# Optimization experiments

Measured on AMD Instinct MI355X. Metric: run time of the kernel, lower is better.

Reference implementation:

```python
import jax, jax.numpy as jnp
import numpy as np

NEG = -10000.0  # fp16-safe mask value, as in the torch module


def prelu(x, a):
    # nn.PReLU() default: single learnable slope shared across channels
    return jnp.where(x >= 0, x, a * x)


def setup_inputs() -> dict:
    key = jax.random.key(0)
    ks = jax.random.split(key, 9)
    B, L, D = 2048, 200, 128
    H1, H2 = 256, 128
    query = jax.random.normal(ks[0], (B, D), dtype=jnp.float32)
    keys = jax.random.normal(ks[1], (B, L, D), dtype=jnp.float32)
    mask = jax.random.randint(ks[2], (B, L), 0, 2, dtype=jnp.int32)
    s1 = 1.0 / np.sqrt(4 * D)
    s2 = 1.0 / np.sqrt(H1)
    s3 = 1.0 / np.sqrt(H2)
    W1 = jax.random.uniform(ks[3], (H1, 4 * D), minval=-s1, maxval=s1, dtype=jnp.float32)
    b1 = jax.random.uniform(ks[4], (H1,), minval=-s1, maxval=s1, dtype=jnp.float32)
    W2 = jax.random.uniform(ks[5], (H2, H1), minval=-s2, maxval=s2, dtype=jnp.float32)
    b2 = jax.random.uniform(ks[6], (H2,), minval=-s2, maxval=s2, dtype=jnp.float32)
    W3 = jax.random.uniform(ks[7], (1, H2), minval=-s3, maxval=s3, dtype=jnp.float32)
    b3 = jax.random.uniform(ks[8], (1,), minval=-s3, maxval=s3, dtype=jnp.float32)
    a1 = jnp.asarray(0.25, dtype=jnp.float32)  # PReLU init
    a2 = jnp.asarray(0.25, dtype=jnp.float32)
    return {"query": query, "keys": keys, "mask": mask,
            "W1": W1, "b1": b1, "a1": a1, "W2": W2, "b2": b2, "a2": a2,
            "W3": W3, "b3": b3}


def reference(query, keys, mask, W1, b1, a1, W2, b2, a2, W3, b3):
    B, L, D = keys.shape
    q = jnp.broadcast_to(query[:, None, :], (B, L, D))
    # [B, L, 4D] concat feature (query, key, diff, product)
    att_in = jnp.concatenate([q, keys, q - keys, q * keys], axis=-1)
    h = prelu(jnp.einsum('blf,hf->blh', att_in, W1) + b1, a1)
    h = prelu(jnp.einsum('blh,gh->blg', h, W2) + b2, a2)
    scores = (jnp.einsum('blg,og->blo', h, W3) + b3)[..., 0]  # [B, L]
    scores = jnp.where(mask == 0, NEG, scores)
    w = jax.nn.softmax(scores, axis=-1)
    w = jnp.where(mask == 0, 0.0, w)
    # weighted sum over history -> user interest [B, D]
    return jnp.einsum('bl,bld->bd', w, keys)
```

## Files before the change

kernel.cpp:

```cpp
#include <hip/hip_runtime.h>
#include <hip/hip_bf16.h>
#include <cstdint>

#define NEGV (-10000.0f)

typedef short bf16x8 __attribute__((ext_vector_type(8)));
typedef short bf16x4 __attribute__((ext_vector_type(4)));
typedef float f32x4 __attribute__((ext_vector_type(4)));

__device__ __forceinline__ short f2bf(float f) {
  union { float f; uint32_t u; } v; v.f = f;
  uint32_t u = v.u + 0x7fffu + ((v.u >> 16) & 1u);
  return (short)(u >> 16);
}
__device__ __forceinline__ float b2f(short s) {
  union { uint32_t u; float f; } v; v.u = ((uint32_t)(uint16_t)s) << 16;
  return v.f;
}
__device__ __forceinline__ uint32_t pk2(float lo, float hi) {
  union { __hip_bfloat162 h2; uint32_t u; } cv;
  cv.h2.x = __float2bfloat16(lo);
  cv.h2.y = __float2bfloat16(hi);
  return cv.u;
}

__global__ void prep_weights(const float* __restrict__ W1, const float* __restrict__ W2,
                             short* __restrict__ Wk, short* __restrict__ Wd,
                             short* __restrict__ W2b) {
  int idx = blockIdx.x * 256 + threadIdx.x;
  if (idx < 32768) {
    int h = idx >> 7, d = idx & 127;
    Wk[idx] = f2bf(W1[h * 512 + 128 + d] - W1[h * 512 + 256 + d]);
  } else if (idx < 65536) {
    int i = idx - 32768;
    int h = i >> 7, d = i & 127;
    Wd[i] = f2bf(W1[h * 512 + 384 + d]);
  } else {
    int i = idx - 65536;
    W2b[i] = f2bf(W2[i]);
  }
}

__global__ void prep_u(const float* __restrict__ query, const float* __restrict__ W1,
                       const float* __restrict__ b1, float* __restrict__ U) {
  __shared__ float q8[8][128];
  int tid = threadIdx.x;
  int b0 = blockIdx.x * 8;
  for (int i = tid; i < 1024; i += 256)
    q8[i >> 7][i & 127] = query[(size_t)(b0 + (i >> 7)) * 128 + (i & 127)];
  __syncthreads();
  int h = tid;
  const float4* w0 = (const float4*)(W1 + (size_t)h * 512);
  const float4* w1 = (const float4*)(W1 + (size_t)h * 512 + 256);
  float acc[8];
  float bb = b1[h];
#pragma unroll
  for (int i = 0; i < 8; ++i) acc[i] = bb;
  for (int d4 = 0; d4 < 32; ++d4) {
    float4 wa = w0[d4], wb = w1[d4];
    float wv0 = wa.x + wb.x, wv1 = wa.y + wb.y, wv2 = wa.z + wb.z, wv3 = wa.w + wb.w;
#pragma unroll
    for (int i = 0; i < 8; ++i) {
      float4 qv = ((const float4*)q8[i])[d4];
      acc[i] += wv0 * qv.x + wv1 * qv.y + wv2 * qv.z + wv3 * qv.w;
    }
  }
#pragma unroll
  for (int i = 0; i < 8; ++i) U[(size_t)(b0 + i) * 256 + h] = acc[i];
}

__global__ __launch_bounds__(256, 2) void din_scores(
    const float* __restrict__ query, const float* __restrict__ keys,
    const float* __restrict__ b2p, const float* __restrict__ a1p,
    const float* __restrict__ a2p, const float* __restrict__ W3,
    const float* __restrict__ U, const short* __restrict__ Wk,
    const short* __restrict__ Wd, const short* __restrict__ W2b,
    float* __restrict__ scores_g) {
  __shared__ short Kt[2][16 * 128];
  __shared__ short H1[2][16 * 256];
  __shared__ float wred[4][208];
  __shared__ float Ul[256];
  __shared__ float b2l[128];
  __shared__ float w3l[128];

  const int tid = threadIdx.x;
  const int b = blockIdx.x;
  const int lane = tid & 63, wid = tid >> 6;
  const int lr = lane & 15, lg = lane >> 4;

  const float a1 = a1p[0], a2 = a2p[0];

  Ul[tid] = U[(size_t)b * 256 + tid];
  if (tid < 128) { b2l[tid] = b2p[tid]; w3l[tid] = W3[tid]; }

  bf16x8 mf[4][4];
  {
    const float* qrow = query + (size_t)b * 128;
#pragma unroll
    for (int nt = 0; nt < 4; ++nt) {
      int h = wid * 64 + nt * 16 + lr;
#pragma unroll
      for (int ks = 0; ks < 4; ++ks) {
        int d0 = ks * 32 + lg * 8;
        bf16x8 wk = *(const bf16x8*)(Wk + h * 128 + d0);
        bf16x8 wd = *(const bf16x8*)(Wd + h * 128 + d0);
        float4 q0 = *(const float4*)(qrow + d0);
        float4 q1 = *(const float4*)(qrow + d0 + 4);
        float qv[8] = {q0.x, q0.y, q0.z, q0.w, q1.x, q1.y, q1.z, q1.w};
        float mv[8];
#pragma unroll
        for (int j = 0; j < 8; ++j) mv[j] = b2f(wk[j]) + b2f(wd[j]) * qv[j];
        union { bf16x8 v; uint32_t u[4]; } mm;
#pragma unroll
        for (int j = 0; j < 4; ++j) mm.u[j] = pk2(mv[2 * j], mv[2 * j + 1]);
        mf[nt][ks] = mm.v;
      }
    }
  }
  bf16x8 w2f[2][8];
#pragma unroll
  for (int nt2 = 0; nt2 < 2; ++nt2) {
    int g = wid * 32 + nt2 * 16 + lr;
#pragma unroll
    for (int ks = 0; ks < 8; ++ks)
      w2f[nt2][ks] = *(const bf16x8*)(W2b + g * 256 + ks * 32 + lg * 8);
  }

  const int srow = tid >> 4;
  const int scol = (tid & 15) * 8;
  const int ssw = (srow & 7) << 3;

  {
    const float4* kp4 = (const float4*)(keys + ((size_t)b * 200 + srow) * 128 + scol);
    float4 s0 = kp4[0], s1 = kp4[1];
    union { bf16x8 v; uint32_t u[4]; } w;
    w.u[0] = pk2(s0.x, s0.y); w.u[1] = pk2(s0.z, s0.w);
    w.u[2] = pk2(s1.x, s1.y); w.u[3] = pk2(s1.z, s1.w);
    *(bf16x8*)(&Kt[0][srow * 128 + (scol ^ ssw)]) = w.v;
  }
  __syncthreads();

  for (int t = 0; t < 13; ++t) {
    const int buf = t & 1;

    float4 st0, st1;
    if (t < 12) {
      int gl = (t + 1) * 16 + srow;
      st0 = st1 = make_float4(0.f, 0.f, 0.f, 0.f);
      if (gl < 200) {
        const float4* kp4 = (const float4*)(keys + ((size_t)b * 200 + gl) * 128 + scol);
        st0 = kp4[0]; st1 = kp4[1];
      }
    }

    const int sw = (lr & 7) << 3;
    bf16x8 kf[4];
#pragma unroll
    for (int ks = 0; ks < 4; ++ks)
      kf[ks] = *(const bf16x8*)(&Kt[buf][lr * 128 + ((ks * 32 + lg * 8) ^ sw)]);
    f32x4 acc[4];
#pragma unroll
    for (int nt = 0; nt < 4; ++nt)
#pragma unroll
      for (int r = 0; r < 4; ++r) acc[nt][r] = Ul[wid * 64 + nt * 16 + lg * 4 + r];
    __builtin_amdgcn_s_setprio(1);
#pragma unroll
    for (int ks = 0; ks < 4; ++ks)
#pragma unroll
      for (int nt = 0; nt < 4; ++nt)
        acc[nt] = __builtin_amdgcn_mfma_f32_16x16x32_bf16(mf[nt][ks], kf[ks], acc[nt], 0, 0, 0);
    __builtin_amdgcn_s_setprio(0);
    short* h1b = H1[buf];
#pragma unroll
    for (int nt = 0; nt < 4; ++nt) {
      float v0 = acc[nt][0], v1 = acc[nt][1], v2 = acc[nt][2], v3 = acc[nt][3];
      v0 = (v0 >= 0.f) ? v0 : a1 * v0;
      v1 = (v1 >= 0.f) ? v1 : a1 * v1;
      v2 = (v2 >= 0.f) ? v2 : a1 * v2;
      v3 = (v3 >= 0.f) ? v3 : a1 * v3;
      union { bf16x4 v; uint32_t u[2]; } hh;
      hh.u[0] = pk2(v0, v1); hh.u[1] = pk2(v2, v3);
      int h0 = wid * 64 + nt * 16 + lg * 4;
      *(bf16x4*)(&h1b[lr * 256 + (h0 ^ sw)]) = hh.v;
    }

    if (t < 12) {
      union { bf16x8 v; uint32_t u[4]; } w;
      w.u[0] = pk2(st0.x, st0.y); w.u[1] = pk2(st0.z, st0.w);
      w.u[2] = pk2(st1.x, st1.y); w.u[3] = pk2(st1.z, st1.w);
      *(bf16x8*)(&Kt[buf ^ 1][srow * 128 + (scol ^ ssw)]) = w.v;
    }
    __syncthreads();

    f32x4 acc2[2];
#pragma unroll
    for (int nt2 = 0; nt2 < 2; ++nt2)
#pragma unroll
      for (int r = 0; r < 4; ++r) acc2[nt2][r] = b2l[wid * 32 + nt2 * 16 + lg * 4 + r];
    __builtin_amdgcn_s_setprio(1);
#pragma unroll
    for (int ks = 0; ks < 8; ++ks) {
      bf16x8 hf = *(const bf16x8*)(&h1b[lr * 256 + ((ks * 32 + lg * 8) ^ sw)]);
      acc2[0] = __builtin_amdgcn_mfma_f32_16x16x32_bf16(w2f[0][ks], hf, acc2[0], 0, 0, 0);
      acc2[1] = __builtin_amdgcn_mfma_f32_16x16x32_bf16(w2f[1][ks], hf, acc2[1], 0, 0, 0);
    }
    __builtin_amdgcn_s_setprio(0);
    float s = 0.f;
#pragma unroll
    for (int nt2 = 0; nt2 < 2; ++nt2)
#pragma unroll
      for (int r = 0; r < 4; ++r) {
        float v = acc2[nt2][r];
        v = (v >= 0.f) ? v : a2 * v;
        s += v * w3l[wid * 32 + nt2 * 16 + lg * 4 + r];
      }
    s += __shfl_xor(s, 16);
    s += __shfl_xor(s, 32);
    if (lg == 0) wred[wid][t * 16 + lr] = s;
  }
  __syncthreads();

  if (tid < 200) {
    float s = wred[0][tid] + wred[1][tid] + wred[2][tid] + wred[3][tid];
    scores_g[(size_t)b * 200 + tid] = s;
  }
}

__global__ __launch_bounds__(256) void din_wsum(
    const float* __restrict__ keys, const int* __restrict__ mask,
    const float* __restrict__ scores_g, float* __restrict__ out) {
  __shared__ float wl[208];
  __shared__ float red[8];
  __shared__ float opart[8][128];

  const int tid = threadIdx.x;
  const int b = blockIdx.x;
  const int lane = tid & 63, wid = tid >> 6;

  float val = NEGV;
  int mk = 0;
  if (tid < 200) {
    mk = mask[(size_t)b * 200 + tid];
    val = mk ? scores_g[(size_t)b * 200 + tid] : NEGV;
  }
  float m = val;
#pragma unroll
  for (int off = 1; off < 64; off <<= 1) m = fmaxf(m, __shfl_xor(m, off));
  if (lane == 0) red[wid] = m;
  __syncthreads();
  float smax = fmaxf(fmaxf(red[0], red[1]), fmaxf(red[2], red[3]));
  float pex = (tid < 200 && mk) ? __expf(val - smax) : 0.f;
  float s = pex;
#pragma unroll
  for (int off = 1; off < 64; off <<= 1) s += __shfl_xor(s, off);
  if (lane == 0) red[4 + wid] = s;
  __syncthreads();
  float ssum = red[4] + red[5] + red[6] + red[7];
  float winv = (ssum > 0.f) ? 1.f / ssum : 0.f;
  if (tid < 208) wl[tid] = (tid < 200) ? pex * winv : 0.f;
  __syncthreads();

  {
    const int d4 = (tid & 31) << 2;
    const int slice = tid >> 5;
    float ax = 0.f, ay = 0.f, az = 0.f, aw = 0.f;
    for (int l = slice; l < 200; l += 8) {
      float wv = wl[l];
      float4 kv = *(const float4*)(keys + ((size_t)b * 200 + l) * 128 + d4);
      ax += wv * kv.x; ay += wv * kv.y; az += wv * kv.z; aw += wv * kv.w;
    }
    *(float4*)(&opart[slice][d4]) = make_float4(ax, ay, az, aw);
  }
  __syncthreads();
  if (tid < 128) {
    float acc = 0.f;
#pragma unroll
    for (int i = 0; i < 8; ++i) acc += opart[i][tid];
    out[(size_t)b * 128 + tid] = acc;
  }
}

extern "C" void kernel_launch(void* const* d_in, const int* in_sizes, int n_in,
                              void* d_out, int out_size, void* d_ws, size_t ws_size,
                              hipStream_t stream) {
  const float* query = (const float*)d_in[0];
  const float* keys  = (const float*)d_in[1];
  const int*   maskp = (const int*)d_in[2];
  const float* W1    = (const float*)d_in[3];
  const float* b1    = (const float*)d_in[4];
  const float* a1    = (const float*)d_in[5];
  const float* W2    = (const float*)d_in[6];
  const float* b2    = (const float*)d_in[7];
  const float* a2    = (const float*)d_in[8];
  const float* W3    = (const float*)d_in[9];
  float* out = (float*)d_out;

  float* U        = (float*)d_ws;
  short* Wk       = (short*)((char*)d_ws + 2097152);
  short* Wd       = Wk + 32768;
  short* W2b      = Wd + 32768;
  float* scores_g = (float*)((char*)d_ws + 2097152 + 196608);

  prep_weights<<<384, 256, 0, stream>>>(W1, W2, Wk, Wd, W2b);
  prep_u<<<256, 256, 0, stream>>>(query, W1, b1, U);
  din_scores<<<2048, 256, 0, stream>>>(query, keys, b2, a1, a2, W3,
                                       U, Wk, Wd, W2b, scores_g);
  din_wsum<<<2048, 256, 0, stream>>>(keys, maskp, scores_g, out);
}
```

Before: 164.0 us.

## Split din_scores into layer-1 and layer-2 warp groups with software pipelining

The score kernel now runs 1024 threads per block: 8 waves compute the first MLP layer for tile t while 8 other waves compute layer 2 and the score reduction for tile t-1 and stage the next key tile. The two layers overlap across warp-specialized groups, which halves per-wave fragment registers and takes the layer-2 work off the layer-1 critical path. In exchange there is an extra pipeline phase, one barrier per phase across 16 waves, likely lower blocks-per-CU occupancy, and U/b2/W3 are read straight from global memory into registers.

```diff
diff --git a/kernel.cpp b/kernel.cpp
--- a/kernel.cpp
+++ b/kernel.cpp
@@ -69,7 +69,7 @@
   for (int i = 0; i < 8; ++i) U[(size_t)(b0 + i) * 256 + h] = acc[i];
 }
 
-__global__ __launch_bounds__(256, 2) void din_scores(
+__global__ __launch_bounds__(1024) void din_scores(
     const float* __restrict__ query, const float* __restrict__ keys,
     const float* __restrict__ b2p, const float* __restrict__ a1p,
     const float* __restrict__ a2p, const float* __restrict__ W3,
@@ -78,27 +78,25 @@
     float* __restrict__ scores_g) {
   __shared__ short Kt[2][16 * 128];
   __shared__ short H1[2][16 * 256];
-  __shared__ float wred[4][208];
-  __shared__ float Ul[256];
-  __shared__ float b2l[128];
-  __shared__ float w3l[128];
+  __shared__ float wred[8][208];
 
   const int tid = threadIdx.x;
   const int b = blockIdx.x;
   const int lane = tid & 63, wid = tid >> 6;
   const int lr = lane & 15, lg = lane >> 4;
-
-  const float a1 = a1p[0], a2 = a2p[0];
-
-  Ul[tid] = U[(size_t)b * 256 + tid];
-  if (tid < 128) { b2l[tid] = b2p[tid]; w3l[tid] = W3[tid]; }
-
-  bf16x8 mf[4][4];
-  {
+  const bool isG1 = wid < 8;
+
+  bf16x8 frag[8];
+  f32x4 accA, accB;
+  float uv0[4], uv1[4];
+  float alpha;
+
+  if (isG1) {
+    alpha = a1p[0];
     const float* qrow = query + (size_t)b * 128;
 #pragma unroll
-    for (int nt = 0; nt < 4; ++nt) {
-      int h = wid * 64 + nt * 16 + lr;
+    for (int nt = 0; nt < 2; ++nt) {
+      int h = wid * 32 + nt * 16 + lr;
 #pragma unroll
       for (int ks = 0; ks < 4; ++ks) {
         int d0 = ks * 32 + lg * 8;
@@ -113,115 +111,123 @@
         union { bf16x8 v; uint32_t u[4]; } mm;
 #pragma unroll
         for (int j = 0; j < 4; ++j) mm.u[j] = pk2(mv[2 * j], mv[2 * j + 1]);
-        mf[nt][ks] = mm.v;
+        frag[nt * 4 + ks] = mm.v;
       }
     }
-  }
-  bf16x8 w2f[2][8];
-#pragma unroll
-  for (int nt2 = 0; nt2 < 2; ++nt2) {
-    int g = wid * 32 + nt2 * 16 + lr;
+#pragma unroll
+    for (int r = 0; r < 4; ++r) {
+      uv0[r] = U[(size_t)b * 256 + wid * 32 + lg * 4 + r];
+      uv1[r] = U[(size_t)b * 256 + wid * 32 + 16 + lg * 4 + r];
+    }
+  } else {
+    alpha = a2p[0];
+    int g = (wid - 8) * 16 + lr;
 #pragma unroll
     for (int ks = 0; ks < 8; ++ks)
-      w2f[nt2][ks] = *(const bf16x8*)(W2b + g * 256 + ks * 32 + lg * 8);
-  }
-
-  const int srow = tid >> 4;
-  const int scol = (tid & 15) * 8;
+      frag[ks] = *(const bf16x8*)(W2b + g * 256 + ks * 32 + lg * 8);
+#pragma unroll
+    for (int r = 0; r < 4; ++r) {
+      int gg = (wid - 8) * 16 + lg * 4 + r;
+      uv0[r] = b2p[gg];
+      uv1[r] = W3[gg];
+    }
+  }
+
+  const int j = tid - 512;
+  const int srow = j >> 5;
+  const int scol = (j & 31) * 4;
   const int ssw = (srow & 7) << 3;
 
-  {
-    const float4* kp4 = (const float4*)(keys + ((size_t)b * 200 + srow) * 128 + scol);
-    float4 s0 = kp4[0], s1 = kp4[1];
-    union { bf16x8 v; uint32_t u[4]; } w;
-    w.u[0] = pk2(s0.x, s0.y); w.u[1] = pk2(s0.z, s0.w);
-    w.u[2] = pk2(s1.x, s1.y); w.u[3] = pk2(s1.z, s1.w);
-    *(bf16x8*)(&Kt[0][srow * 128 + (scol ^ ssw)]) = w.v;
-  }
-  __syncthreads();
-
-  for (int t = 0; t < 13; ++t) {
-    const int buf = t & 1;
-
-    float4 st0, st1;
-    if (t < 12) {
-      int gl = (t + 1) * 16 + srow;
-      st0 = st1 = make_float4(0.f, 0.f, 0.f, 0.f);
-      if (gl < 200) {
-        const float4* kp4 = (const float4*)(keys + ((size_t)b * 200 + gl) * 128 + scol);
-        st0 = kp4[0]; st1 = kp4[1];
+  if (!isG1) {
+    float4 st = *(const float4*)(keys + ((size_t)b * 200 + srow) * 128 + scol);
+    union { bf16x4 v; uint32_t u[2]; } w;
+    w.u[0] = pk2(st.x, st.y); w.u[1] = pk2(st.z, st.w);
+    *(bf16x4*)(&Kt[0][srow * 128 + (scol ^ ssw)]) = w.v;
+  }
+  __syncthreads();
+
+  const int sw = (lr & 7) << 3;
+
+  for (int ph = 0; ph < 14; ++ph) {
+    const int buf = ph & 1;
+
+    float4 st;
+    bool sv = false;
+    if (!isG1 && ph < 12) {
+      int gl = (ph + 1) * 16 + srow;
+      st = make_float4(0.f, 0.f, 0.f, 0.f);
+      sv = true;
+      if (gl < 200) st = *(const float4*)(keys + ((size_t)b * 200 + gl) * 128 + scol);
+    }
+
+    if (isG1) {
+      if (ph < 13) {
+        bf16x8 kf[4];
+#pragma unroll
+        for (int ks = 0; ks < 4; ++ks)
+          kf[ks] = *(const bf16x8*)(&Kt[buf][lr * 128 + ((ks * 32 + lg * 8) ^ sw)]);
+#pragma unroll
+        for (int r = 0; r < 4; ++r) { accA[r] = uv0[r]; accB[r] = uv1[r]; }
+        __builtin_amdgcn_s_setprio(1);
+#pragma unroll
+        for (int ks = 0; ks < 4; ++ks) {
+          accA = __builtin_amdgcn_mfma_f32_16x16x32_bf16(frag[ks], kf[ks], accA, 0, 0, 0);
+          accB = __builtin_amdgcn_mfma_f32_16x16x32_bf16(frag[4 + ks], kf[ks], accB, 0, 0, 0);
+        }
+        __builtin_amdgcn_s_setprio(0);
+        float v0, v1, v2, v3;
+        union { bf16x4 v; uint32_t u[2]; } hh;
+        v0 = accA[0]; v1 = accA[1]; v2 = accA[2]; v3 = accA[3];
+        v0 = (v0 >= 0.f) ? v0 : alpha * v0;
+        v1 = (v1 >= 0.f) ? v1 : alpha * v1;
+        v2 = (v2 >= 0.f) ? v2 : alpha * v2;
+        v3 = (v3 >= 0.f) ? v3 : alpha * v3;
+        hh.u[0] = pk2(v0, v1); hh.u[1] = pk2(v2, v3);
+        *(bf16x4*)(&H1[buf][lr * 256 + ((wid * 32 + lg * 4) ^ sw)]) = hh.v;
+        v0 = accB[0]; v1 = accB[1]; v2 = accB[2]; v3 = accB[3];
+        v0 = (v0 >= 0.f) ? v0 : alpha * v0;
+        v1 = (v1 >= 0.f) ? v1 : alpha * v1;
+        v2 = (v2 >= 0.f) ? v2 : alpha * v2;
+        v3 = (v3 >= 0.f) ? v3 : alpha * v3;
+        hh.u[0] = pk2(v0, v1); hh.u[1] = pk2(v2, v3);
+        *(bf16x4*)(&H1[buf][lr * 256 + ((wid * 32 + 16 + lg * 4) ^ sw)]) = hh.v;
       }
-    }
-
-    const int sw = (lr & 7) << 3;
-    bf16x8 kf[4];
-#pragma unroll
-    for (int ks = 0; ks < 4; ++ks)
-      kf[ks] = *(const bf16x8*)(&Kt[buf][lr * 128 + ((ks * 32 + lg * 8) ^ sw)]);
-    f32x4 acc[4];
-#pragma unroll
-    for (int nt = 0; nt < 4; ++nt)
-#pragma unroll
-      for (int r = 0; r < 4; ++r) acc[nt][r] = Ul[wid * 64 + nt * 16 + lg * 4 + r];
-    __builtin_amdgcn_s_setprio(1);
-#pragma unroll
-    for (int ks = 0; ks < 4; ++ks)
-#pragma unroll
-      for (int nt = 0; nt < 4; ++nt)
-        acc[nt] = __builtin_amdgcn_mfma_f32_16x16x32_bf16(mf[nt][ks], kf[ks], acc[nt], 0, 0, 0);
-    __builtin_amdgcn_s_setprio(0);
-    short* h1b = H1[buf];
-#pragma unroll
-    for (int nt = 0; nt < 4; ++nt) {
-      float v0 = acc[nt][0], v1 = acc[nt][1], v2 = acc[nt][2], v3 = acc[nt][3];
-      v0 = (v0 >= 0.f) ? v0 : a1 * v0;
-      v1 = (v1 >= 0.f) ? v1 : a1 * v1;
-      v2 = (v2 >= 0.f) ? v2 : a1 * v2;
-      v3 = (v3 >= 0.f) ? v3 : a1 * v3;
-      union { bf16x4 v; uint32_t u[2]; } hh;
-      hh.u[0] = pk2(v0, v1); hh.u[1] = pk2(v2, v3);
-      int h0 = wid * 64 + nt * 16 + lg * 4;
-      *(bf16x4*)(&h1b[lr * 256 + (h0 ^ sw)]) = hh.v;
-    }
-
-    if (t < 12) {
-      union { bf16x8 v; uint32_t u[4]; } w;
-      w.u[0] = pk2(st0.x, st0.y); w.u[1] = pk2(st0.z, st0.w);
-      w.u[2] = pk2(st1.x, st1.y); w.u[3] = pk2(st1.z, st1.w);
-      *(bf16x8*)(&Kt[buf ^ 1][srow * 128 + (scol ^ ssw)]) = w.v;
+    } else {
+      if (ph >= 1) {
+#pragma unroll
+        for (int r = 0; r < 4; ++r) accA[r] = uv0[r];
+        const short* h1b = H1[buf ^ 1];
+        __builtin_amdgcn_s_setprio(1);
+#pragma unroll
+        for (int ks = 0; ks < 8; ++ks) {
+          bf16x8 hf = *(const bf16x8*)(&h1b[lr * 256 + ((ks * 32 + lg * 8) ^ sw)]);
+          accA = __builtin_amdgcn_mfma_f32_16x16x32_bf16(frag[ks], hf, accA, 0, 0, 0);
+        }
+        __builtin_amdgcn_s_setprio(0);
+        float s = 0.f;
+#pragma unroll
+        for (int r = 0; r < 4; ++r) {
+          float v = accA[r];
+          v = (v >= 0.f) ? v : alpha * v;
+          s += v * uv1[r];
+        }
+        s += __shfl_xor(s, 16);
+        s += __shfl_xor(s, 32);
+        if (lg == 0) wred[wid - 8][(ph - 1) * 16 + lr] = s;
+      }
+      if (sv) {
+        union { bf16x4 v; uint32_t u[2]; } w;
+        w.u[0] = pk2(st.x, st.y); w.u[1] = pk2(st.z, st.w);
+        *(bf16x4*)(&Kt[buf ^ 1][srow * 128 + (scol ^ ssw)]) = w.v;
+      }
     }
     __syncthreads();
-
-    f32x4 acc2[2];
-#pragma unroll
-    for (int nt2 = 0; nt2 < 2; ++nt2)
-#pragma unroll
-      for (int r = 0; r < 4; ++r) acc2[nt2][r] = b2l[wid * 32 + nt2 * 16 + lg * 4 + r];
-    __builtin_amdgcn_s_setprio(1);
-#pragma unroll
-    for (int ks = 0; ks < 8; ++ks) {
-      bf16x8 hf = *(const bf16x8*)(&h1b[lr * 256 + ((ks * 32 + lg * 8) ^ sw)]);
-      acc2[0] = __builtin_amdgcn_mfma_f32_16x16x32_bf16(w2f[0][ks], hf, acc2[0], 0, 0, 0);
-      acc2[1] = __builtin_amdgcn_mfma_f32_16x16x32_bf16(w2f[1][ks], hf, acc2[1], 0, 0, 0);
-    }
-    __builtin_amdgcn_s_setprio(0);
+  }
+
+  if (tid < 200) {
     float s = 0.f;
 #pragma unroll
-    for (int nt2 = 0; nt2 < 2; ++nt2)
-#pragma unroll
-      for (int r = 0; r < 4; ++r) {
-        float v = acc2[nt2][r];
-        v = (v >= 0.f) ? v : a2 * v;
-        s += v * w3l[wid * 32 + nt2 * 16 + lg * 4 + r];
-      }
-    s += __shfl_xor(s, 16);
-    s += __shfl_xor(s, 32);
-    if (lg == 0) wred[wid][t * 16 + lr] = s;
-  }
-  __syncthreads();
-
-  if (tid < 200) {
-    float s = wred[0][tid] + wred[1][tid] + wred[2][tid] + wred[3][tid];
+    for (int w = 0; w < 8; ++w) s += wred[w][tid];
     scores_g[(size_t)b * 200 + tid] = s;
   }
 }
@@ -303,7 +309,7 @@
 
   prep_weights<<<384, 256, 0, stream>>>(W1, W2, Wk, Wd, W2b);
   prep_u<<<256, 256, 0, stream>>>(query, W1, b1, U);
-  din_scores<<<2048, 256, 0, stream>>>(query, keys, b2, a1, a2, W3,
-                                       U, Wk, Wd, W2b, scores_g);
+  din_scores<<<2048, 1024, 0, stream>>>(query, keys, b2, a1, a2, W3,
+                                        U, Wk, Wd, W2b, scores_g);
   din_wsum<<<2048, 256, 0, stream>>>(keys, maskp, scores_g, out);
 }
```

Result: slower. 188.3 us (+14.8%).
